# Optimization experiments

Hardware: AMD Instinct MI355X
Metric: run time of the kernel (lower is better)

## Reference

```python
import jax, jax.numpy as jnp
import numpy as np

HIDDEN = 896
INTER = 2560
N_EXPERTS = 16
TOP_K = 4


def setup_inputs() -> dict:
    key = jax.random.key(0)
    ks = jax.random.split(key, 9)
    s = lambda fan_in: 1.0 / np.sqrt(fan_in)
    x = jax.random.normal(ks[0], (2, 1024, HIDDEN), dtype=jnp.float32)
    router_w = jax.random.normal(ks[1], (HIDDEN, N_EXPERTS), dtype=jnp.float32) * s(HIDDEN)
    # routed experts, stacked: y = x @ W (equivalent to nn.Linear with W.T)
    Wg = jax.random.normal(ks[2], (N_EXPERTS, HIDDEN, INTER), dtype=jnp.float32) * s(HIDDEN)
    Wu = jax.random.normal(ks[3], (N_EXPERTS, HIDDEN, INTER), dtype=jnp.float32) * s(HIDDEN)
    Wd = jax.random.normal(ks[4], (N_EXPERTS, INTER, HIDDEN), dtype=jnp.float32) * s(INTER)
    # single shared expert
    Sg = jax.random.normal(ks[5], (HIDDEN, INTER), dtype=jnp.float32) * s(HIDDEN)
    Su = jax.random.normal(ks[6], (HIDDEN, INTER), dtype=jnp.float32) * s(HIDDEN)
    Sd = jax.random.normal(ks[7], (INTER, HIDDEN), dtype=jnp.float32) * s(INTER)
    return {"x": x, "router_w": router_w, "Wg": Wg, "Wu": Wu, "Wd": Wd,
            "Sg": Sg, "Su": Su, "Sd": Sd}


def reference(x, router_w, Wg, Wu, Wd, Sg, Su, Sd):
    B, N, D = x.shape
    xf = x.reshape(-1, D)  # [T, D]

    # shared expert (all tokens): SwiGLU
    shared = (jax.nn.silu(xf @ Sg) * (xf @ Su)) @ Sd  # [T, D]

    # router: softmax -> top-k -> renormalize
    logits = xf @ router_w                      # [T, E]
    probs = jax.nn.softmax(logits, axis=-1)
    top_v, top_i = jax.lax.top_k(probs, TOP_K)  # [T, K]
    w = top_v / (top_v.sum(axis=-1, keepdims=True) + 1e-8)

    # load-balance loss
    one_hot = jax.nn.one_hot(top_i, N_EXPERTS, dtype=probs.dtype)  # [T, K, E]
    f = one_hot.sum(axis=1).mean(axis=0)   # fraction routed per expert
    P = probs.mean(axis=0)                 # mean router prob per expert
    balance_loss = N_EXPERTS * (f * P).sum()

    # dense-dispatch combine weights [T, E] (zero for unselected experts)
    combine = (w[..., None] * one_hot).sum(axis=1)  # [T, E]

    # all-expert SwiGLU, combined with per-token routing weights
    g = jnp.einsum('td,edi->tei', xf, Wg)
    u = jnp.einsum('td,edi->tei', xf, Wu)
    h = jax.nn.silu(g) * u                          # [T, E, I]
    routed = jnp.einsum('tei,eid,te->td', h, Wd, combine)

    out = (routed + shared).reshape(B, N, D)
    return out, balance_loss
```

## Files before the change

### kernel.cpp

```cpp
#include <hip/hip_runtime.h>
#include <hip/hip_bf16.h>


#define T_TOK 2048
#define DIM   896
#define INTERN 2560
#define NEXP  16
#define TOPK  4
#define MT    64
#define IC    256

#define SLOTGU ((size_t)80 * 56 * 512)
#define SLOTD  ((size_t)28 * 160 * 512)

typedef __attribute__((ext_vector_type(8)))  __bf16 bf16x8;
typedef __attribute__((ext_vector_type(4)))  __bf16 bf16x4;
typedef __attribute__((ext_vector_type(16))) float  f32x16;

__device__ __forceinline__ void panel_barrier() {
  asm volatile("s_waitcnt lgkmcnt(0)" ::: "memory");
  __builtin_amdgcn_s_barrier();
  __builtin_amdgcn_sched_barrier(0);
}

__global__ void router_k(const float* __restrict__ x, const float* __restrict__ rw,
                         int* __restrict__ cnt, float* __restrict__ Pacc,
                         float* __restrict__ facc, int* __restrict__ tok,
                         float* __restrict__ wts) {
  int lane = threadIdx.x & 63;
  int t = blockIdx.x * 4 + (threadIdx.x >> 6);
  const float* xr = x + (size_t)t * DIM;

  float acc[NEXP];
#pragma unroll
  for (int e = 0; e < NEXP; ++e) acc[e] = 0.f;
  for (int i = 0; i < DIM / 64; ++i) {
    int d = i * 64 + lane;
    float xv = xr[d];
    const float* r = rw + d * NEXP;
#pragma unroll
    for (int e = 0; e < NEXP; ++e) acc[e] = fmaf(xv, r[e], acc[e]);
  }
#pragma unroll
  for (int e = 0; e < NEXP; ++e) {
    float v = acc[e];
    v += __shfl_xor(v, 32); v += __shfl_xor(v, 16); v += __shfl_xor(v, 8);
    v += __shfl_xor(v, 4);  v += __shfl_xor(v, 2);  v += __shfl_xor(v, 1);
    acc[e] = v;
  }
  float m = acc[0];
#pragma unroll
  for (int e = 1; e < NEXP; ++e) m = fmaxf(m, acc[e]);
  float p[NEXP]; float s = 0.f;
#pragma unroll
  for (int e = 0; e < NEXP; ++e) { p[e] = __expf(acc[e] - m); s += p[e]; }
  float is = 1.f / s;
#pragma unroll
  for (int e = 0; e < NEXP; ++e) p[e] *= is;

  float pc[NEXP];
#pragma unroll
  for (int e = 0; e < NEXP; ++e) pc[e] = p[e];
  int sels[TOPK]; float svs[TOPK]; float s4 = 0.f;
#pragma unroll
  for (int k = 0; k < TOPK; ++k) {
    int best = 0; float bv = pc[0];
#pragma unroll
    for (int e = 1; e < NEXP; ++e) { if (pc[e] > bv) { bv = pc[e]; best = e; } }
    sels[k] = best; svs[k] = bv; s4 += bv;
#pragma unroll
    for (int e = 0; e < NEXP; ++e) { if (e == best) pc[e] = -1.f; }
  }
  float inv = 1.f / (s4 + 1e-8f);

  if (lane < NEXP) atomicAdd(&Pacc[lane], p[lane] * (1.f / T_TOK));
  if (lane < TOPK) {
    int e = sels[lane]; float w = svs[lane] * inv;
    atomicAdd(&facc[e], 1.f / T_TOK);
    int pos = atomicAdd(&cnt[e], 1);
    tok[e * T_TOK + pos] = t;
    wts[e * T_TOK + pos] = w;
  }
}

__global__ void loss_k(const float* __restrict__ Pacc, const float* __restrict__ facc,
                       const int* __restrict__ cnt, int* __restrict__ offs,
                       float* __restrict__ dst) {
  if (threadIdx.x == 0) {
    float s = 0.f;
    for (int e = 0; e < NEXP; ++e) s += Pacc[e] * facc[e];
    *dst = (float)NEXP * s;
    int o = 0;
    for (int e = 0; e < NEXP; ++e) { offs[e] = o; o += cnt[e]; }
    offs[NEXP] = o;
  }
}

__global__ __launch_bounds__(256, 8) void packall_k(
    const float* __restrict__ Wg, const float* __restrict__ Sg,
    __hip_bfloat16* __restrict__ PG,
    const float* __restrict__ Wu, const float* __restrict__ Su,
    __hip_bfloat16* __restrict__ PU,
    const float* __restrict__ Wd, const float* __restrict__ Sd,
    __hip_bfloat16* __restrict__ PD) {
  int bid = blockIdx.x;
  int which = bid / 9520;
  int r = bid % 9520;
  int z = r / 560, rr = r % 560;
  int K, N, kt, nt;
  const float *srcE, *srcS; __hip_bfloat16* dst;
  if (which < 2) {
    K = DIM; N = INTERN; kt = rr % 14; nt = rr / 14;
    srcE = which ? Wu : Wg; srcS = which ? Su : Sg; dst = which ? PU : PG;
  } else {
    K = INTERN; N = DIM; kt = rr % 40; nt = rr / 40;
    srcE = Wd; srcS = Sd; dst = PD;
  }
  const float* src = (z < NEXP) ? srcE + (size_t)z * K * N : srcS;
  __hip_bfloat16* d = dst + (size_t)z * ((size_t)(K >> 4) * (N >> 5) * 512);

  __shared__ float tile[64][65];
  int tid = threadIdx.x;
  int r0 = tid >> 4, c4 = (tid & 15) << 2;
  const float* s = src + (size_t)(kt * 64) * N + nt * 64;
#pragma unroll
  for (int it = 0; it < 4; ++it) {
    int rw_ = r0 + 16 * it;
    float4 v = *reinterpret_cast<const float4*>(s + (size_t)rw_ * N + c4);
    tile[rw_][c4] = v.x; tile[rw_][c4 + 1] = v.y;
    tile[rw_][c4 + 2] = v.z; tile[rw_][c4 + 3] = v.w;
  }
  __syncthreads();
  int lane = tid & 63, h5 = lane >> 5, c31 = lane & 31;
  int KS = K >> 4;
#pragma unroll
  for (int it = 0; it < 2; ++it) {
    int cc = (tid >> 6) + 4 * it;
    int nbl = cc >> 2, ksl = cc & 3;
    bf16x8 v;
#pragma unroll
    for (int e = 0; e < 8; ++e)
      v[e] = (__bf16)tile[ksl * 16 + 8 * h5 + e][nbl * 32 + c31];
    size_t n_blk = (size_t)nt * 2 + nbl, ks = (size_t)kt * 4 + ksl;
    *reinterpret_cast<bf16x8*>(d + ((n_blk * KS + ks) * 64 + lane) * 8) = v;
  }
}

__global__ __launch_bounds__(512, 4) void h4_k(
    const float* __restrict__ x, const int* __restrict__ cnt,
    const int* __restrict__ offs, const int* __restrict__ tok,
    const __hip_bfloat16* __restrict__ PG, const __hip_bfloat16* __restrict__ PU,
    __hip_bfloat16* __restrict__ H) {
  int bid = blockIdx.x;
  int ch = bid / 544, r_ = bid % 544;
  int g = r_ % 17, tile = r_ / 17;
  int M = (g < NEXP) ? cnt[g] : T_TOK;
  int m0 = tile * MT;
  if (m0 >= M) return;

  __shared__ int rows_s[MT];
  __shared__ __align__(16) char xph[32768];
  char (*xp)[16384] = reinterpret_cast<char (*)[16384]>(xph);
  char* hb = xph;

  int tid = threadIdx.x;
  if (tid < MT) {
    if (g < NEXP) {
      int i = m0 + tid;
      rows_s[tid] = tok[g * T_TOK + ((i < M) ? i : m0)];
    } else rows_s[tid] = m0 + tid;
  }
  __syncthreads();

  int wv = tid >> 6, lane = tid & 63;
  int h5 = lane >> 5, c31 = lane & 31;

  int srow = tid >> 3, sc8 = tid & 7;
  const float* xr = x + (size_t)rows_s[srow] * DIM;
  int sswz = (srow & 7) << 4;

#define LDX(p, j) (*reinterpret_cast<const float4*>(xr + (p) * 128 + (sc8 + 8 * (j)) * 4))
#define STX(pb, j, v) { bf16x4 _b; _b[0]=(__bf16)(v).x; _b[1]=(__bf16)(v).y; \
    _b[2]=(__bf16)(v).z; _b[3]=(__bf16)(v).w; \
    *reinterpret_cast<bf16x4*>(&xp[pb][(srow * 256 + sc8 * 8 + 64 * (j)) ^ sswz]) = _b; }
#define XF(pb, row, ksl) (*reinterpret_cast<const bf16x8*>( \
    &xp[pb][((row) * 256 + (ksl) * 32 + h5 * 16) ^ (((row) & 7) << 4)]))

  int slot = (g < NEXP) ? g : NEXP;
  const __hip_bfloat16* bg = PG + (size_t)slot * SLOTGU +
      ((size_t)(ch * 8 + wv) * 56) * 512 + lane * 8;
  const __hip_bfloat16* bu = PU + (size_t)slot * SLOTGU +
      ((size_t)(ch * 8 + wv) * 56) * 512 + lane * 8;

  bf16x8 g0 = *reinterpret_cast<const bf16x8*>(bg);
  bf16x8 g1 = *reinterpret_cast<const bf16x8*>(bg + 512);
  bf16x8 g2 = *reinterpret_cast<const bf16x8*>(bg + 1024);
  bf16x8 g3 = *reinterpret_cast<const bf16x8*>(bg + 1536);
  bf16x8 u0 = *reinterpret_cast<const bf16x8*>(bu);
  bf16x8 u1 = *reinterpret_cast<const bf16x8*>(bu + 512);
  bf16x8 u2 = *reinterpret_cast<const bf16x8*>(bu + 1024);
  bf16x8 u3 = *reinterpret_cast<const bf16x8*>(bu + 1536);

  {
    float4 a0 = LDX(0, 0), a1 = LDX(0, 1), a2 = LDX(0, 2), a3 = LDX(0, 3);
    STX(0, 0, a0) STX(0, 1, a1) STX(0, 2, a2) STX(0, 3, a3)
  }
  panel_barrier();

  f32x16 ag0, ag1, au0, au1;
#pragma unroll
  for (int r = 0; r < 16; ++r) { ag0[r] = 0.f; ag1[r] = 0.f; au0[r] = 0.f; au1[r] = 0.f; }

#define STEP(S, GB, UB) { \
    bf16x8 xa = XF(pb, c31, S), xb = XF(pb, c31 + 32, S); \
    ag0 = __builtin_amdgcn_mfma_f32_32x32x16_bf16(GB, xa, ag0, 0, 0, 0); \
    ag1 = __builtin_amdgcn_mfma_f32_32x32x16_bf16(GB, xb, ag1, 0, 0, 0); \
    au0 = __builtin_amdgcn_mfma_f32_32x32x16_bf16(UB, xa, au0, 0, 0, 0); \
    au1 = __builtin_amdgcn_mfma_f32_32x32x16_bf16(UB, xb, au1, 0, 0, 0); \
    int nk = 8 * p + (S) + 4; if (nk >= 56) nk = 0; \
    GB = *reinterpret_cast<const bf16x8*>(bg + (size_t)nk * 512); \
    UB = *reinterpret_cast<const bf16x8*>(bu + (size_t)nk * 512); }

  float4 s0, s1, s2, s3;
  for (int p = 0; p < 7; ++p) {
    int pb = p & 1;
    if (p < 6) { s0 = LDX(p + 1, 0); s1 = LDX(p + 1, 1); }
    STEP(0, g0, u0) STEP(1, g1, u1) STEP(2, g2, u2)
    if (p < 6) {
      STX(pb ^ 1, 0, s0) STX(pb ^ 1, 1, s1)
      s2 = LDX(p + 1, 2); s3 = LDX(p + 1, 3);
    }
    STEP(3, g3, u3) STEP(4, g0, u0) STEP(5, g1, u1)
    if (p < 6) { STX(pb ^ 1, 2, s2) STX(pb ^ 1, 3, s3) }
    STEP(6, g2, u2) STEP(7, g3, u3)
    panel_barrier();
  }
#undef STEP

#pragma unroll
  for (int mh = 0; mh < 2; ++mh) {
    int tokr = c31 + 32 * mh;
#pragma unroll
    for (int q = 0; q < 4; ++q) {
      bf16x4 hq;
#pragma unroll
      for (int j = 0; j < 4; ++j) {
        float gg = mh ? ag1[4 * q + j] : ag0[4 * q + j];
        float uu = mh ? au1[4 * q + j] : au0[4 * q + j];
        hq[j] = (__bf16)(gg / (1.f + __expf(-gg)) * uu);
      }
      int i0 = wv * 32 + 8 * q + 4 * h5;
      int byte = (tokr * 512 + i0 * 2) ^ ((tokr & 7) << 4);
      *reinterpret_cast<bf16x4*>(&hb[byte]) = hq;
    }
  }
  panel_barrier();

  if (g == NEXP || m0 + srow < M) {
    int slotr = offs[g] + m0 + srow;
    __hip_bfloat16* hrow = H + (size_t)slotr * INTERN + ch * IC + sc8 * 32;
#pragma unroll
    for (int qq = 0; qq < 4; ++qq) {
      int byte = (srow * 512 + sc8 * 64 + qq * 16) ^ sswz;
      *reinterpret_cast<bf16x8*>(hrow + qq * 8) =
          *reinterpret_cast<const bf16x8*>(&hb[byte]);
    }
  }
#undef LDX
#undef STX
#undef XF
}

__global__ __launch_bounds__(512, 4) void g24_k(
    const int* __restrict__ cnt, const int* __restrict__ offs,
    const int* __restrict__ tok, const float* __restrict__ wts,
    const __hip_bfloat16* __restrict__ H,
    const __hip_bfloat16* __restrict__ PD, float* __restrict__ out) {
  int bid = blockIdx.x;
  int ns = bid / 544, r_ = bid % 544;
  int g = r_ % 17, tile = r_ / 17;
  int M = (g < NEXP) ? cnt[g] : T_TOK;
  int m0 = tile * MT;
  if (m0 >= M) return;

  __shared__ int rows_s[MT];
  __shared__ float w_s[MT];
  __shared__ __align__(16) char hp[2][16384];

  int tid = threadIdx.x;
  if (tid < MT) {
    if (g < NEXP) {
      int i = m0 + tid; bool v = i < M;
      rows_s[tid] = tok[g * T_TOK + (v ? i : m0)];
      w_s[tid]   = v ? wts[g * T_TOK + i] : 0.f;
    } else { rows_s[tid] = m0 + tid; w_s[tid] = 1.f; }
  }
  __syncthreads();

  int wv = tid >> 6, lane = tid & 63, h5 = lane >> 5, c31 = lane & 31;
  int mh = wv & 1, ng = wv >> 1;
  int col = ns * 128 + ng * 32 + c31;

  int slot = (g < NEXP) ? g : NEXP;
  const __hip_bfloat16* bd = PD + (size_t)slot * SLOTD +
      ((size_t)(ns * 4 + ng) * 160) * 512 + lane * 8;

  int slot0 = offs[g] + m0;
  const __hip_bfloat16* Hb = H + (size_t)slot0 * INTERN;

  int srow = tid >> 3, sc8 = tid & 7;
  const __hip_bfloat16* hr = Hb + (size_t)srow * INTERN + sc8 * 16;
  int sswz = (srow & 7) << 4;

  bf16x8 w0 = *reinterpret_cast<const bf16x8*>(bd);
  bf16x8 w1 = *reinterpret_cast<const bf16x8*>(bd + 512);
  bf16x8 w2 = *reinterpret_cast<const bf16x8*>(bd + 1024);
  bf16x8 w3 = *reinterpret_cast<const bf16x8*>(bd + 1536);
  bf16x8 w4 = *reinterpret_cast<const bf16x8*>(bd + 2048);
  bf16x8 w5 = *reinterpret_cast<const bf16x8*>(bd + 2560);
  bf16x8 w6 = *reinterpret_cast<const bf16x8*>(bd + 3072);
  bf16x8 w7 = *reinterpret_cast<const bf16x8*>(bd + 3584);

  bf16x8 t0 = *reinterpret_cast<const bf16x8*>(hr);
  bf16x8 t1 = *reinterpret_cast<const bf16x8*>(hr + 8);
  {
    int b0 = srow * 256 + sc8 * 32;
    *reinterpret_cast<bf16x8*>(&hp[0][b0 ^ sswz]) = t0;
    *reinterpret_cast<bf16x8*>(&hp[0][(b0 + 16) ^ sswz]) = t1;
  }
  panel_barrier();

  f32x16 o;
#pragma unroll
  for (int r = 0; r < 16; ++r) o[r] = 0.f;

  int arow = mh * 32 + c31;
  int aswz = (arow & 7) << 4;

#define G2STEP(KSL, WB) { \
    bf16x8 hf = *reinterpret_cast<const bf16x8*>( \
        &hp[pb][(arow * 256 + (KSL) * 32 + h5 * 16) ^ aswz]); \
    o = __builtin_amdgcn_mfma_f32_32x32x16_bf16(hf, WB, o, 0, 0, 0); \
    int tn = 8 * p + (KSL) + 8; if (tn >= 160) tn -= 160; \
    WB = *reinterpret_cast<const bf16x8*>(bd + (size_t)tn * 512); }

  for (int p = 0; p < 20; ++p) {
    int pb = p & 1;
    if (p < 19) {
      t0 = *reinterpret_cast<const bf16x8*>(hr + (p + 1) * 128);
      t1 = *reinterpret_cast<const bf16x8*>(hr + (p + 1) * 128 + 8);
    }
    G2STEP(0, w0) G2STEP(1, w1) G2STEP(2, w2) G2STEP(3, w3)
    G2STEP(4, w4) G2STEP(5, w5) G2STEP(6, w6) G2STEP(7, w7)
    if (p < 19) {
      int b0 = srow * 256 + sc8 * 32;
      *reinterpret_cast<bf16x8*>(&hp[pb ^ 1][b0 ^ sswz]) = t0;
      *reinterpret_cast<bf16x8*>(&hp[pb ^ 1][(b0 + 16) ^ sswz]) = t1;
    }
    panel_barrier();
  }
#undef G2STEP

#pragma unroll
  for (int r = 0; r < 16; ++r) {
    int row = (r & 3) + 8 * (r >> 2) + 4 * h5 + 32 * mh;
    atomicAdd(&out[(size_t)rows_s[row] * DIM + col], o[r] * w_s[row]);
  }
}

extern "C" void kernel_launch(void* const* d_in, const int* in_sizes, int n_in,
                              void* d_out, int out_size, void* d_ws, size_t ws_size,
                              hipStream_t stream) {
  const float* x  = (const float*)d_in[0];
  const float* rw = (const float*)d_in[1];
  const float* Wg = (const float*)d_in[2];
  const float* Wu = (const float*)d_in[3];
  const float* Wd = (const float*)d_in[4];
  const float* Sg = (const float*)d_in[5];
  const float* Su = (const float*)d_in[6];
  const float* Sd = (const float*)d_in[7];
  float* out = (float*)d_out;

  char* ws = (char*)d_ws;
  int*   cnt  = (int*)ws;
  float* Pacc = (float*)(ws + 64);
  float* facc = (float*)(ws + 128);
  int*   offs = (int*)(ws + 192);
  int*   tok  = (int*)(ws + 320);
  float* wts  = (float*)(ws + 320 + 131072);
  const size_t H_OFF = 262656;
  __hip_bfloat16* H = (__hip_bfloat16*)(ws + H_OFF);
  const size_t H_BYTES = (size_t)(2 * T_TOK * TOPK + T_TOK) * INTERN * 2;

  const size_t PG_OFF = H_OFF + H_BYTES;
  const size_t PBYTES = (size_t)17 * SLOTGU * 2;
  const size_t PU_OFF = PG_OFF + PBYTES;
  const size_t PD_OFF = PU_OFF + PBYTES;
  __hip_bfloat16* PG = (__hip_bfloat16*)(ws + PG_OFF);
  __hip_bfloat16* PU = (__hip_bfloat16*)(ws + PU_OFF);
  __hip_bfloat16* PD = (__hip_bfloat16*)(ws + PD_OFF);

  hipMemsetAsync(d_ws, 0, 320, stream);
  hipMemsetAsync(d_out, 0, (size_t)(T_TOK * DIM + 1) * sizeof(float), stream);

  router_k<<<T_TOK / 4, 256, 0, stream>>>(x, rw, cnt, Pacc, facc, tok, wts);
  loss_k<<<1, 64, 0, stream>>>(Pacc, facc, cnt, offs, out + (size_t)T_TOK * DIM);
  packall_k<<<28560, 256, 0, stream>>>(Wg, Sg, PG, Wu, Su, PU, Wd, Sd, PD);
  h4_k<<<5440, 512, 0, stream>>>(x, cnt, offs, tok, PG, PU, H);
  g24_k<<<3808, 512, 0, stream>>>(cnt, offs, tok, wts, H, PD, out);
}
```

Measured before the change: 637.4 us.

## Use persistent blocks pulling from per-bucket work lists for expert GEMMs

Replaces the fixed grids of the gate/up and down-projection kernels, where many blocks exit early for empty tiles, with 1024 persistent blocks. Each block pops items from one of 8 precomputed work lists via an atomic counter. loss_k builds the lists so each bucket holds two experts plus a share of the shared-expert tiles, ordered by column chunk to encourage weight reuse in cache. This removes the launch cost of empty blocks and is meant to balance load across CUs, at the price of a serial single-thread list build and per-item atomic and barrier overhead.

```diff
diff --git a/kernel.cpp b/kernel.cpp
--- a/kernel.cpp
+++ b/kernel.cpp
@@ -85,7 +85,9 @@
 
 __global__ void loss_k(const float* __restrict__ Pacc, const float* __restrict__ facc,
                        const int* __restrict__ cnt, int* __restrict__ offs,
-                       float* __restrict__ dst) {
+                       float* __restrict__ dst,
+                       int* __restrict__ wcnt_h, int* __restrict__ wl_h,
+                       int* __restrict__ wcnt_g, int* __restrict__ wl_g) {
   if (threadIdx.x == 0) {
     float s = 0.f;
     for (int e = 0; e < NEXP; ++e) s += Pacc[e] * facc[e];
@@ -93,6 +95,24 @@
     int o = 0;
     for (int e = 0; e < NEXP; ++e) { offs[e] = o; o += cnt[e]; }
     offs[NEXP] = o;
+    for (int b = 0; b < 8; ++b) {
+      int K0 = (cnt[b] + MT - 1) >> 6;
+      int K1 = (cnt[b + 8] + MT - 1) >> 6;
+      int n = 0;
+      for (int ch = 0; ch < 10; ++ch) {
+        for (int t = 0; t < K0; ++t) wl_h[b * 1024 + n++] = (ch << 16) | (b << 8) | t;
+        for (int t = 0; t < K1; ++t) wl_h[b * 1024 + n++] = (ch << 16) | ((b + 8) << 8) | t;
+        for (int j = 0; j < 4; ++j)  wl_h[b * 1024 + n++] = (ch << 16) | (NEXP << 8) | (b + 8 * j);
+      }
+      wcnt_h[b] = n;
+      n = 0;
+      for (int ns = 0; ns < 7; ++ns) {
+        for (int t = 0; t < K0; ++t) wl_g[b * 512 + n++] = (ns << 16) | (b << 8) | t;
+        for (int t = 0; t < K1; ++t) wl_g[b * 512 + n++] = (ns << 16) | ((b + 8) << 8) | t;
+        for (int j = 0; j < 4; ++j)  wl_g[b * 512 + n++] = (ns << 16) | (NEXP << 8) | (b + 8 * j);
+      }
+      wcnt_g[b] = n;
+    }
   }
 }
 
@@ -146,38 +166,47 @@
   }
 }
 
-__global__ __launch_bounds__(512, 4) void h4_k(
+__global__ __launch_bounds__(512, 4) void h4p_k(
     const float* __restrict__ x, const int* __restrict__ cnt,
     const int* __restrict__ offs, const int* __restrict__ tok,
     const __hip_bfloat16* __restrict__ PG, const __hip_bfloat16* __restrict__ PU,
-    __hip_bfloat16* __restrict__ H) {
-  int bid = blockIdx.x;
-  int ch = bid / 544, r_ = bid % 544;
-  int g = r_ % 17, tile = r_ / 17;
-  int M = (g < NEXP) ? cnt[g] : T_TOK;
-  int m0 = tile * MT;
-  if (m0 >= M) return;
-
+    __hip_bfloat16* __restrict__ H,
+    int* __restrict__ pop, const int* __restrict__ wcnt,
+    const int* __restrict__ wl) {
+  int bkt = blockIdx.x & 7;
+  __shared__ int item_s;
   __shared__ int rows_s[MT];
   __shared__ __align__(16) char xph[32768];
   char (*xp)[16384] = reinterpret_cast<char (*)[16384]>(xph);
   char* hb = xph;
 
   int tid = threadIdx.x;
-  if (tid < MT) {
-    if (g < NEXP) {
-      int i = m0 + tid;
-      rows_s[tid] = tok[g * T_TOK + ((i < M) ? i : m0)];
-    } else rows_s[tid] = m0 + tid;
-  }
-  __syncthreads();
-
   int wv = tid >> 6, lane = tid & 63;
   int h5 = lane >> 5, c31 = lane & 31;
-
   int srow = tid >> 3, sc8 = tid & 7;
-  const float* xr = x + (size_t)rows_s[srow] * DIM;
   int sswz = (srow & 7) << 4;
+
+  for (;;) {
+    if (tid == 0) {
+      int i = atomicAdd(&pop[bkt], 1);
+      item_s = (i < wcnt[bkt]) ? wl[bkt * 1024 + i] : -1;
+    }
+    __syncthreads();
+    int item = item_s;
+    if (item < 0) break;
+    int ch = item >> 16, g = (item >> 8) & 255, tile = item & 255;
+    int M = (g < NEXP) ? cnt[g] : T_TOK;
+    int m0 = tile * MT;
+
+    if (tid < MT) {
+      if (g < NEXP) {
+        int i = m0 + tid;
+        rows_s[tid] = tok[g * T_TOK + ((i < M) ? i : m0)];
+      } else rows_s[tid] = m0 + tid;
+    }
+    __syncthreads();
+
+    const float* xr = x + (size_t)rows_s[srow] * DIM;
 
 #define LDX(p, j) (*reinterpret_cast<const float4*>(xr + (p) * 128 + (sc8 + 8 * (j)) * 4))
 #define STX(pb, j, v) { bf16x4 _b; _b[0]=(__bf16)(v).x; _b[1]=(__bf16)(v).y; \
@@ -186,30 +215,30 @@
 #define XF(pb, row, ksl) (*reinterpret_cast<const bf16x8*>( \
     &xp[pb][((row) * 256 + (ksl) * 32 + h5 * 16) ^ (((row) & 7) << 4)]))
 
-  int slot = (g < NEXP) ? g : NEXP;
-  const __hip_bfloat16* bg = PG + (size_t)slot * SLOTGU +
-      ((size_t)(ch * 8 + wv) * 56) * 512 + lane * 8;
-  const __hip_bfloat16* bu = PU + (size_t)slot * SLOTGU +
-      ((size_t)(ch * 8 + wv) * 56) * 512 + lane * 8;
-
-  bf16x8 g0 = *reinterpret_cast<const bf16x8*>(bg);
-  bf16x8 g1 = *reinterpret_cast<const bf16x8*>(bg + 512);
-  bf16x8 g2 = *reinterpret_cast<const bf16x8*>(bg + 1024);
-  bf16x8 g3 = *reinterpret_cast<const bf16x8*>(bg + 1536);
-  bf16x8 u0 = *reinterpret_cast<const bf16x8*>(bu);
-  bf16x8 u1 = *reinterpret_cast<const bf16x8*>(bu + 512);
-  bf16x8 u2 = *reinterpret_cast<const bf16x8*>(bu + 1024);
-  bf16x8 u3 = *reinterpret_cast<const bf16x8*>(bu + 1536);
-
-  {
-    float4 a0 = LDX(0, 0), a1 = LDX(0, 1), a2 = LDX(0, 2), a3 = LDX(0, 3);
-    STX(0, 0, a0) STX(0, 1, a1) STX(0, 2, a2) STX(0, 3, a3)
-  }
-  panel_barrier();
-
-  f32x16 ag0, ag1, au0, au1;
-#pragma unroll
-  for (int r = 0; r < 16; ++r) { ag0[r] = 0.f; ag1[r] = 0.f; au0[r] = 0.f; au1[r] = 0.f; }
+    int slot = (g < NEXP) ? g : NEXP;
+    const __hip_bfloat16* bg = PG + (size_t)slot * SLOTGU +
+        ((size_t)(ch * 8 + wv) * 56) * 512 + lane * 8;
+    const __hip_bfloat16* bu = PU + (size_t)slot * SLOTGU +
+        ((size_t)(ch * 8 + wv) * 56) * 512 + lane * 8;
+
+    bf16x8 g0 = *reinterpret_cast<const bf16x8*>(bg);
+    bf16x8 g1 = *reinterpret_cast<const bf16x8*>(bg + 512);
+    bf16x8 g2 = *reinterpret_cast<const bf16x8*>(bg + 1024);
+    bf16x8 g3 = *reinterpret_cast<const bf16x8*>(bg + 1536);
+    bf16x8 u0 = *reinterpret_cast<const bf16x8*>(bu);
+    bf16x8 u1 = *reinterpret_cast<const bf16x8*>(bu + 512);
+    bf16x8 u2 = *reinterpret_cast<const bf16x8*>(bu + 1024);
+    bf16x8 u3 = *reinterpret_cast<const bf16x8*>(bu + 1536);
+
+    {
+      float4 a0 = LDX(0, 0), a1 = LDX(0, 1), a2 = LDX(0, 2), a3 = LDX(0, 3);
+      STX(0, 0, a0) STX(0, 1, a1) STX(0, 2, a2) STX(0, 3, a3)
+    }
+    panel_barrier();
+
+    f32x16 ag0, ag1, au0, au1;
+#pragma unroll
+    for (int r = 0; r < 16; ++r) { ag0[r] = 0.f; ag1[r] = 0.f; au0[r] = 0.f; au1[r] = 0.f; }
 
 #define STEP(S, GB, UB) { \
     bf16x8 xa = XF(pb, c31, S), xb = XF(pb, c31 + 32, S); \
@@ -221,121 +250,128 @@
     GB = *reinterpret_cast<const bf16x8*>(bg + (size_t)nk * 512); \
     UB = *reinterpret_cast<const bf16x8*>(bu + (size_t)nk * 512); }
 
-  float4 s0, s1, s2, s3;
-  for (int p = 0; p < 7; ++p) {
-    int pb = p & 1;
-    if (p < 6) { s0 = LDX(p + 1, 0); s1 = LDX(p + 1, 1); }
-    STEP(0, g0, u0) STEP(1, g1, u1) STEP(2, g2, u2)
-    if (p < 6) {
-      STX(pb ^ 1, 0, s0) STX(pb ^ 1, 1, s1)
-      s2 = LDX(p + 1, 2); s3 = LDX(p + 1, 3);
-    }
-    STEP(3, g3, u3) STEP(4, g0, u0) STEP(5, g1, u1)
-    if (p < 6) { STX(pb ^ 1, 2, s2) STX(pb ^ 1, 3, s3) }
-    STEP(6, g2, u2) STEP(7, g3, u3)
+    float4 s0, s1, s2, s3;
+    for (int p = 0; p < 7; ++p) {
+      int pb = p & 1;
+      if (p < 6) { s0 = LDX(p + 1, 0); s1 = LDX(p + 1, 1); }
+      STEP(0, g0, u0) STEP(1, g1, u1) STEP(2, g2, u2)
+      if (p < 6) {
+        STX(pb ^ 1, 0, s0) STX(pb ^ 1, 1, s1)
+        s2 = LDX(p + 1, 2); s3 = LDX(p + 1, 3);
+      }
+      STEP(3, g3, u3) STEP(4, g0, u0) STEP(5, g1, u1)
+      if (p < 6) { STX(pb ^ 1, 2, s2) STX(pb ^ 1, 3, s3) }
+      STEP(6, g2, u2) STEP(7, g3, u3)
+      panel_barrier();
+    }
+#undef STEP
+
+#pragma unroll
+    for (int mh = 0; mh < 2; ++mh) {
+      int tokr = c31 + 32 * mh;
+#pragma unroll
+      for (int q = 0; q < 4; ++q) {
+        bf16x4 hq;
+#pragma unroll
+        for (int j = 0; j < 4; ++j) {
+          float gg = mh ? ag1[4 * q + j] : ag0[4 * q + j];
+          float uu = mh ? au1[4 * q + j] : au0[4 * q + j];
+          hq[j] = (__bf16)(gg / (1.f + __expf(-gg)) * uu);
+        }
+        int i0 = wv * 32 + 8 * q + 4 * h5;
+        int byte = (tokr * 512 + i0 * 2) ^ ((tokr & 7) << 4);
+        *reinterpret_cast<bf16x4*>(&hb[byte]) = hq;
+      }
+    }
     panel_barrier();
-  }
-#undef STEP
-
-#pragma unroll
-  for (int mh = 0; mh < 2; ++mh) {
-    int tokr = c31 + 32 * mh;
-#pragma unroll
-    for (int q = 0; q < 4; ++q) {
-      bf16x4 hq;
-#pragma unroll
-      for (int j = 0; j < 4; ++j) {
-        float gg = mh ? ag1[4 * q + j] : ag0[4 * q + j];
-        float uu = mh ? au1[4 * q + j] : au0[4 * q + j];
-        hq[j] = (__bf16)(gg / (1.f + __expf(-gg)) * uu);
-      }
-      int i0 = wv * 32 + 8 * q + 4 * h5;
-      int byte = (tokr * 512 + i0 * 2) ^ ((tokr & 7) << 4);
-      *reinterpret_cast<bf16x4*>(&hb[byte]) = hq;
-    }
-  }
-  panel_barrier();
-
-  if (g == NEXP || m0 + srow < M) {
-    int slotr = offs[g] + m0 + srow;
-    __hip_bfloat16* hrow = H + (size_t)slotr * INTERN + ch * IC + sc8 * 32;
-#pragma unroll
-    for (int qq = 0; qq < 4; ++qq) {
-      int byte = (srow * 512 + sc8 * 64 + qq * 16) ^ sswz;
-      *reinterpret_cast<bf16x8*>(hrow + qq * 8) =
-          *reinterpret_cast<const bf16x8*>(&hb[byte]);
-    }
-  }
+
+    if (g == NEXP || m0 + srow < M) {
+      int slotr = offs[g] + m0 + srow;
+      __hip_bfloat16* hrow = H + (size_t)slotr * INTERN + ch * IC + sc8 * 32;
+#pragma unroll
+      for (int qq = 0; qq < 4; ++qq) {
+        int byte = (srow * 512 + sc8 * 64 + qq * 16) ^ sswz;
+        *reinterpret_cast<bf16x8*>(hrow + qq * 8) =
+            *reinterpret_cast<const bf16x8*>(&hb[byte]);
+      }
+    }
 #undef LDX
 #undef STX
 #undef XF
-}
-
-__global__ __launch_bounds__(512, 4) void g24_k(
+  }
+}
+
+__global__ __launch_bounds__(512, 4) void g24p_k(
     const int* __restrict__ cnt, const int* __restrict__ offs,
     const int* __restrict__ tok, const float* __restrict__ wts,
     const __hip_bfloat16* __restrict__ H,
-    const __hip_bfloat16* __restrict__ PD, float* __restrict__ out) {
-  int bid = blockIdx.x;
-  int ns = bid / 544, r_ = bid % 544;
-  int g = r_ % 17, tile = r_ / 17;
-  int M = (g < NEXP) ? cnt[g] : T_TOK;
-  int m0 = tile * MT;
-  if (m0 >= M) return;
-
+    const __hip_bfloat16* __restrict__ PD, float* __restrict__ out,
+    int* __restrict__ pop, const int* __restrict__ wcnt,
+    const int* __restrict__ wl) {
+  int bkt = blockIdx.x & 7;
+  __shared__ int item_s;
   __shared__ int rows_s[MT];
   __shared__ float w_s[MT];
   __shared__ __align__(16) char hp[2][16384];
 
   int tid = threadIdx.x;
-  if (tid < MT) {
-    if (g < NEXP) {
-      int i = m0 + tid; bool v = i < M;
-      rows_s[tid] = tok[g * T_TOK + (v ? i : m0)];
-      w_s[tid]   = v ? wts[g * T_TOK + i] : 0.f;
-    } else { rows_s[tid] = m0 + tid; w_s[tid] = 1.f; }
-  }
-  __syncthreads();
-
   int wv = tid >> 6, lane = tid & 63, h5 = lane >> 5, c31 = lane & 31;
   int mh = wv & 1, ng = wv >> 1;
-  int col = ns * 128 + ng * 32 + c31;
-
-  int slot = (g < NEXP) ? g : NEXP;
-  const __hip_bfloat16* bd = PD + (size_t)slot * SLOTD +
-      ((size_t)(ns * 4 + ng) * 160) * 512 + lane * 8;
-
-  int slot0 = offs[g] + m0;
-  const __hip_bfloat16* Hb = H + (size_t)slot0 * INTERN;
-
   int srow = tid >> 3, sc8 = tid & 7;
-  const __hip_bfloat16* hr = Hb + (size_t)srow * INTERN + sc8 * 16;
   int sswz = (srow & 7) << 4;
-
-  bf16x8 w0 = *reinterpret_cast<const bf16x8*>(bd);
-  bf16x8 w1 = *reinterpret_cast<const bf16x8*>(bd + 512);
-  bf16x8 w2 = *reinterpret_cast<const bf16x8*>(bd + 1024);
-  bf16x8 w3 = *reinterpret_cast<const bf16x8*>(bd + 1536);
-  bf16x8 w4 = *reinterpret_cast<const bf16x8*>(bd + 2048);
-  bf16x8 w5 = *reinterpret_cast<const bf16x8*>(bd + 2560);
-  bf16x8 w6 = *reinterpret_cast<const bf16x8*>(bd + 3072);
-  bf16x8 w7 = *reinterpret_cast<const bf16x8*>(bd + 3584);
-
-  bf16x8 t0 = *reinterpret_cast<const bf16x8*>(hr);
-  bf16x8 t1 = *reinterpret_cast<const bf16x8*>(hr + 8);
-  {
-    int b0 = srow * 256 + sc8 * 32;
-    *reinterpret_cast<bf16x8*>(&hp[0][b0 ^ sswz]) = t0;
-    *reinterpret_cast<bf16x8*>(&hp[0][(b0 + 16) ^ sswz]) = t1;
-  }
-  panel_barrier();
-
-  f32x16 o;
-#pragma unroll
-  for (int r = 0; r < 16; ++r) o[r] = 0.f;
-
   int arow = mh * 32 + c31;
   int aswz = (arow & 7) << 4;
+
+  for (;;) {
+    if (tid == 0) {
+      int i = atomicAdd(&pop[bkt], 1);
+      item_s = (i < wcnt[bkt]) ? wl[bkt * 512 + i] : -1;
+    }
+    __syncthreads();
+    int item = item_s;
+    if (item < 0) break;
+    int ns = item >> 16, g = (item >> 8) & 255, tile = item & 255;
+    int M = (g < NEXP) ? cnt[g] : T_TOK;
+    int m0 = tile * MT;
+
+    if (tid < MT) {
+      if (g < NEXP) {
+        int i = m0 + tid; bool v = i < M;
+        rows_s[tid] = tok[g * T_TOK + (v ? i : m0)];
+        w_s[tid]   = v ? wts[g * T_TOK + i] : 0.f;
+      } else { rows_s[tid] = m0 + tid; w_s[tid] = 1.f; }
+    }
+    __syncthreads();
+
+    int col = ns * 128 + ng * 32 + c31;
+    int slot = (g < NEXP) ? g : NEXP;
+    const __hip_bfloat16* bd = PD + (size_t)slot * SLOTD +
+        ((size_t)(ns * 4 + ng) * 160) * 512 + lane * 8;
+
+    int slot0 = offs[g] + m0;
+    const __hip_bfloat16* hr = H + (size_t)(slot0 + srow) * INTERN + sc8 * 16;
+
+    bf16x8 w0 = *reinterpret_cast<const bf16x8*>(bd);
+    bf16x8 w1 = *reinterpret_cast<const bf16x8*>(bd + 512);
+    bf16x8 w2 = *reinterpret_cast<const bf16x8*>(bd + 1024);
+    bf16x8 w3 = *reinterpret_cast<const bf16x8*>(bd + 1536);
+    bf16x8 w4 = *reinterpret_cast<const bf16x8*>(bd + 2048);
+    bf16x8 w5 = *reinterpret_cast<const bf16x8*>(bd + 2560);
+    bf16x8 w6 = *reinterpret_cast<const bf16x8*>(bd + 3072);
+    bf16x8 w7 = *reinterpret_cast<const bf16x8*>(bd + 3584);
+
+    bf16x8 t0 = *reinterpret_cast<const bf16x8*>(hr);
+    bf16x8 t1 = *reinterpret_cast<const bf16x8*>(hr + 8);
+    {
+      int b0 = srow * 256 + sc8 * 32;
+      *reinterpret_cast<bf16x8*>(&hp[0][b0 ^ sswz]) = t0;
+      *reinterpret_cast<bf16x8*>(&hp[0][(b0 + 16) ^ sswz]) = t1;
+    }
+    panel_barrier();
+
+    f32x16 o;
+#pragma unroll
+    for (int r = 0; r < 16; ++r) o[r] = 0.f;
 
 #define G2STEP(KSL, WB) { \
     bf16x8 hf = *reinterpret_cast<const bf16x8*>( \
@@ -344,27 +380,28 @@
     int tn = 8 * p + (KSL) + 8; if (tn >= 160) tn -= 160; \
     WB = *reinterpret_cast<const bf16x8*>(bd + (size_t)tn * 512); }
 
-  for (int p = 0; p < 20; ++p) {
-    int pb = p & 1;
-    if (p < 19) {
-      t0 = *reinterpret_cast<const bf16x8*>(hr + (p + 1) * 128);
-      t1 = *reinterpret_cast<const bf16x8*>(hr + (p + 1) * 128 + 8);
-    }
-    G2STEP(0, w0) G2STEP(1, w1) G2STEP(2, w2) G2STEP(3, w3)
-    G2STEP(4, w4) G2STEP(5, w5) G2STEP(6, w6) G2STEP(7, w7)
-    if (p < 19) {
-      int b0 = srow * 256 + sc8 * 32;
-      *reinterpret_cast<bf16x8*>(&hp[pb ^ 1][b0 ^ sswz]) = t0;
-      *reinterpret_cast<bf16x8*>(&hp[pb ^ 1][(b0 + 16) ^ sswz]) = t1;
-    }
-    panel_barrier();
-  }
+    for (int p = 0; p < 20; ++p) {
+      int pb = p & 1;
+      if (p < 19) {
+        t0 = *reinterpret_cast<const bf16x8*>(hr + (p + 1) * 128);
+        t1 = *reinterpret_cast<const bf16x8*>(hr + (p + 1) * 128 + 8);
+      }
+      G2STEP(0, w0) G2STEP(1, w1) G2STEP(2, w2) G2STEP(3, w3)
+      G2STEP(4, w4) G2STEP(5, w5) G2STEP(6, w6) G2STEP(7, w7)
+      if (p < 19) {
+        int b0 = srow * 256 + sc8 * 32;
+        *reinterpret_cast<bf16x8*>(&hp[pb ^ 1][b0 ^ sswz]) = t0;
+        *reinterpret_cast<bf16x8*>(&hp[pb ^ 1][(b0 + 16) ^ sswz]) = t1;
+      }
+      panel_barrier();
+    }
 #undef G2STEP
 
 #pragma unroll
-  for (int r = 0; r < 16; ++r) {
-    int row = (r & 3) + 8 * (r >> 2) + 4 * h5 + 32 * mh;
-    atomicAdd(&out[(size_t)rows_s[row] * DIM + col], o[r] * w_s[row]);
+    for (int r = 0; r < 16; ++r) {
+      int row = (r & 3) + 8 * (r >> 2) + 4 * h5 + 32 * mh;
+      atomicAdd(&out[(size_t)rows_s[row] * DIM + col], o[r] * w_s[row]);
+    }
   }
 }
 
@@ -382,13 +419,19 @@
   float* out = (float*)d_out;
 
   char* ws = (char*)d_ws;
-  int*   cnt  = (int*)ws;
-  float* Pacc = (float*)(ws + 64);
-  float* facc = (float*)(ws + 128);
-  int*   offs = (int*)(ws + 192);
-  int*   tok  = (int*)(ws + 320);
-  float* wts  = (float*)(ws + 320 + 131072);
-  const size_t H_OFF = 262656;
+  int*   cnt    = (int*)ws;
+  float* Pacc   = (float*)(ws + 64);
+  float* facc   = (float*)(ws + 128);
+  int*   offs   = (int*)(ws + 192);
+  int*   pop_h  = (int*)(ws + 320);
+  int*   pop_g  = (int*)(ws + 352);
+  int*   wcnt_h = (int*)(ws + 384);
+  int*   wcnt_g = (int*)(ws + 416);
+  int*   tok    = (int*)(ws + 512);
+  float* wts    = (float*)(ws + 512 + 131072);
+  int*   wl_h   = (int*)(ws + 262656);
+  int*   wl_g   = (int*)(ws + 295424);
+  const size_t H_OFF = 311808;
   __hip_bfloat16* H = (__hip_bfloat16*)(ws + H_OFF);
   const size_t H_BYTES = (size_t)(2 * T_TOK * TOPK + T_TOK) * INTERN * 2;
 
@@ -400,12 +443,15 @@
   __hip_bfloat16* PU = (__hip_bfloat16*)(ws + PU_OFF);
   __hip_bfloat16* PD = (__hip_bfloat16*)(ws + PD_OFF);
 
-  hipMemsetAsync(d_ws, 0, 320, stream);
+  hipMemsetAsync(d_ws, 0, 448, stream);
   hipMemsetAsync(d_out, 0, (size_t)(T_TOK * DIM + 1) * sizeof(float), stream);
 
   router_k<<<T_TOK / 4, 256, 0, stream>>>(x, rw, cnt, Pacc, facc, tok, wts);
-  loss_k<<<1, 64, 0, stream>>>(Pacc, facc, cnt, offs, out + (size_t)T_TOK * DIM);
+  loss_k<<<1, 64, 0, stream>>>(Pacc, facc, cnt, offs, out + (size_t)T_TOK * DIM,
+                               wcnt_h, wl_h, wcnt_g, wl_g);
   packall_k<<<28560, 256, 0, stream>>>(Wg, Sg, PG, Wu, Su, PU, Wd, Sd, PD);
-  h4_k<<<5440, 512, 0, stream>>>(x, cnt, offs, tok, PG, PU, H);
-  g24_k<<<3808, 512, 0, stream>>>(cnt, offs, tok, wts, H, PD, out);
-}
+  h4p_k<<<1024, 512, 0, stream>>>(x, cnt, offs, tok, PG, PU, H,
+                                  pop_h, wcnt_h, wl_h);
+  g24p_k<<<1024, 512, 0, stream>>>(cnt, offs, tok, wts, H, PD, out,
+                                   pop_g, wcnt_g, wl_g);
+}
```

Result: faster. 598.9 us (-6.0%).
